# Kernel tuning notes

Measured on AMD Instinct MI355X. Metric: run time of the kernel, lower is better.

The kernel has to match this reference:

```python
import jax, jax.numpy as jnp
import numpy as np

B, T, I, H, O = 512, 512, 128, 50, 10


def setup_inputs() -> dict:
    key = jax.random.key(0)
    ks = jax.random.split(key, 7)
    return {
        "x": jax.random.normal(ks[0], (B, T, I), dtype=jnp.float32),
        "W_ih": jax.random.normal(ks[1], (4 * H, I), dtype=jnp.float32) * 0.05,
        "W_hh": jax.random.normal(ks[2], (4 * H, H), dtype=jnp.float32) * 0.05,
        "b_ih": jax.random.normal(ks[3], (4 * H,), dtype=jnp.float32) * 0.05,
        "b_hh": jax.random.normal(ks[4], (4 * H,), dtype=jnp.float32) * 0.05,
        "W_fc": jax.random.normal(ks[5], (O, H), dtype=jnp.float32) * 0.05,
        "b_fc": jax.random.normal(ks[6], (O,), dtype=jnp.float32) * 0.05,
    }


def reference(x, W_ih, W_hh, b_ih, b_hh, W_fc, b_fc):
    # Single-layer LSTM (PyTorch gate order i,f,g,o), batch_first, zero init state.
    Bsz = x.shape[0]
    Hd = W_hh.shape[1]
    bias = b_ih + b_hh  # [4H]
    # Precompute input projections for all timesteps: [T, B, 4H]
    x_proj = jnp.einsum('bti,gi->tbg', x, W_ih) + bias

    def step(carry, xp_t):
        h, c = carry  # [B, H] each
        gates = xp_t + h @ W_hh.T  # [B, 4H]
        i, f, g, o = jnp.split(gates, 4, axis=-1)
        i = jax.nn.sigmoid(i)
        f = jax.nn.sigmoid(f)
        g = jnp.tanh(g)
        o = jax.nn.sigmoid(o)
        c = f * c + i * g
        h = o * jnp.tanh(c)
        return (h, c), None

    h0 = jnp.zeros((Bsz, Hd), dtype=x.dtype)
    c0 = jnp.zeros((Bsz, Hd), dtype=x.dtype)
    (h_last, _), _ = jax.lax.scan(step, (h0, c0), x_proj)
    return h_last @ W_fc.T + b_fc  # [B, O]
```

## Files before the change

kernel.cpp:

```cpp
#include <hip/hip_runtime.h>


#define BB 512
#define TT 512
#define II 128
#define HH 50
#define GG 200

typedef _Float16 half2v __attribute__((ext_vector_type(2)));
typedef _Float16 half4v __attribute__((ext_vector_type(4)));
typedef _Float16 half8v __attribute__((ext_vector_type(8)));
typedef float float4v __attribute__((ext_vector_type(4)));

#if defined(__has_builtin)
#if __has_builtin(__builtin_amdgcn_fdot2)
#define HAVE_FDOT2 1
#endif
#endif

__device__ __forceinline__ float fdot2f(half2v a, half2v b, float c) {
#ifdef HAVE_FDOT2
    return __builtin_amdgcn_fdot2(a, b, c, false);
#else
    return c + (float)a[0] * (float)b[0] + (float)a[1] * (float)b[1];
#endif
}

__device__ __forceinline__ float fsig(float x) {
    return 1.f / (1.f + __expf(-x));
}
__device__ __forceinline__ float ftanh(float x) {
    return 2.f * fsig(2.f * x) - 1.f;
}

__global__ __launch_bounds__(256) void prep_kernel(
    const float* __restrict__ W_ih, const float* __restrict__ W_hh,
    const float* __restrict__ b_ih, const float* __restrict__ b_hh,
    _Float16* __restrict__ wfrags, _Float16* __restrict__ whh16,
    float* __restrict__ biasv)
{
    int idx = blockIdx.x * 256 + threadIdx.x;
    if (idx < 3328) {
        int lane = idx & 63, kc = (idx >> 6) & 3, nt = idx >> 8;
        int gp = nt * 16 + (lane & 15);
        int k0 = kc * 32 + ((lane >> 4) & 3) * 8;
        half8v v;
        if (gp < GG) {
            int u = gp >> 2, j = gp & 3;
            const float* wr = W_ih + (size_t)(j * HH + u) * II + k0;
            #pragma unroll
            for (int q = 0; q < 8; ++q) v[q] = (_Float16)wr[q];
        } else {
            #pragma unroll
            for (int q = 0; q < 8; ++q) v[q] = (_Float16)0.f;
        }
        *(half8v*)(wfrags + (size_t)idx * 8) = v;
    } else if (idx < 3328 + 2800) {
        int r = idx - 3328;
        int g = r / 14, j4 = r % 14;
        #pragma unroll
        for (int j = 0; j < 4; ++j) {
            int hidx = j4 * 4 + j;
            whh16[g * 56 + hidx] = (hidx < HH) ? (_Float16)W_hh[g * HH + hidx]
                                               : (_Float16)0.f;
        }
    } else if (idx < 3328 + 2800 + GG) {
        int gp = idx - 6128;
        int u = gp >> 2, j = gp & 3;
        biasv[gp] = b_ih[j * HH + u] + b_hh[j * HH + u];
    }
}

__global__ __launch_bounds__(256) void xproj_mfma(
    const float* __restrict__ x, const _Float16* __restrict__ wfrags,
    const float* __restrict__ biasv, _Float16* __restrict__ xp16,
    int t0, int ntile)
{
    __shared__ __align__(16) _Float16 wflds[3328 * 8];
    __shared__ __align__(16) _Float16 dtile[64 * GG];
    __shared__ float blds[GG];
    const int tid = threadIdx.x;
    const int b = blockIdx.x;
    const int w = tid >> 6, l = tid & 63;

    for (int s = tid; s < 3328; s += 256)
        *(float4v*)(wflds + (size_t)s * 8) = *(const float4v*)(wfrags + (size_t)s * 8);
    for (int s = tid; s < GG; s += 256) blds[s] = biasv[s];

    const int row = w * 16 + (l & 15);
    const int kq = (l >> 4) & 3;
    const float* xbase = x + ((size_t)b * TT + (size_t)t0 + row) * II + kq * 8;

    float4 f0[4], f1[4];
    #pragma unroll
    for (int kc = 0; kc < 4; ++kc) {
        f0[kc] = *(const float4*)(xbase + kc * 32);
        f1[kc] = *(const float4*)(xbase + kc * 32 + 4);
    }
    __syncthreads();

    const int colb = l & 15, rq = l >> 4;

    for (int tt = 0; tt < ntile; ++tt) {
        half8v a[4];
        #pragma unroll
        for (int kc = 0; kc < 4; ++kc) {
            a[kc][0] = (_Float16)f0[kc].x; a[kc][1] = (_Float16)f0[kc].y;
            a[kc][2] = (_Float16)f0[kc].z; a[kc][3] = (_Float16)f0[kc].w;
            a[kc][4] = (_Float16)f1[kc].x; a[kc][5] = (_Float16)f1[kc].y;
            a[kc][6] = (_Float16)f1[kc].z; a[kc][7] = (_Float16)f1[kc].w;
        }
        if (tt + 1 < ntile) {
            const float* xn = xbase + (size_t)(tt + 1) * 64 * II;
            #pragma unroll
            for (int kc = 0; kc < 4; ++kc) {
                f0[kc] = *(const float4*)(xn + kc * 32);
                f1[kc] = *(const float4*)(xn + kc * 32 + 4);
            }
        }

        float4v acc[13];
        #pragma unroll
        for (int nt = 0; nt < 13; ++nt) acc[nt] = (float4v){0.f, 0.f, 0.f, 0.f};
        #pragma unroll
        for (int kc = 0; kc < 4; ++kc) {
            #pragma unroll
            for (int nt = 0; nt < 13; ++nt) {
                half8v bf = *(const half8v*)(wflds + (size_t)(((nt * 4 + kc) * 64) + l) * 8);
                acc[nt] = __builtin_amdgcn_mfma_f32_16x16x32_f16(a[kc], bf, acc[nt], 0, 0, 0);
            }
        }

        __syncthreads();
        #pragma unroll
        for (int nt = 0; nt < 13; ++nt) {
            int g = nt * 16 + colb;
            if (g < GG) {
                float bs = blds[g];
                #pragma unroll
                for (int reg = 0; reg < 4; ++reg)
                    dtile[(w * 16 + rq * 4 + reg) * GG + g] = (_Float16)(acc[nt][reg] + bs);
            }
        }
        __syncthreads();

        _Float16* outp = xp16 + ((size_t)b * ntile + tt) * 64 * GG;
        #pragma unroll
        for (int it = 0; it < 7; ++it) {
            int idx = it * 256 + tid;
            if (idx < 1600) {
                float4v v = *(const float4v*)(dtile + (size_t)idx * 8);
                *(float4v*)(outp + (size_t)idx * 8) = v;
            }
        }
    }
}

__global__
__attribute__((amdgpu_flat_work_group_size(256, 256)))
__attribute__((amdgpu_waves_per_eu(1, 2)))
void lstm_rec(
    const _Float16* __restrict__ xp16, const _Float16* __restrict__ whh16,
    float* __restrict__ hs, float* __restrict__ cs, int Tc, int first)
{
    __shared__ __align__(16) _Float16 hbuf[56];
    const int b = blockIdx.x;
    const int tid = threadIdx.x;
    const int gp = (tid < GG) ? tid : 197;
    const int u = gp >> 2;
    const int gate = gp & 3;
    const int wrow = gate * HH + u;

    float4v wv[7];
    #pragma unroll
    for (int j = 0; j < 7; ++j)
        wv[j] = *(const float4v*)(whh16 + (size_t)wrow * 56 + j * 8);

    float c = (!first) ? cs[b * HH + u] : 0.f;

    if (tid < 56)
        hbuf[tid] = (tid < HH && !first) ? (_Float16)hs[b * HH + tid]
                                         : (_Float16)0.f;
    __syncthreads();

    const _Float16* xpb = xp16 + (size_t)b * Tc * GG + gp;
    _Float16 xpf = xpb[0];

    float hlast = 0.f;
    for (int t = 0; t < Tc; ++t) {
        int tn = (t + 1 < Tc) ? t + 1 : t;
        _Float16 xnew = xpb[(size_t)tn * GG];

        float4v hv[7];
        #pragma unroll
        for (int j = 0; j < 7; ++j) hv[j] = *(const float4v*)(hbuf + j * 8);

        float a0 = 0.f, a1 = 0.f, a2 = 0.f, a3 = 0.f;
        #pragma unroll
        for (int j = 0; j < 7; ++j) {
            const half2v* hp = (const half2v*)&hv[j];
            const half2v* wp = (const half2v*)&wv[j];
            a0 = fdot2f(hp[0], wp[0], a0);
            a1 = fdot2f(hp[1], wp[1], a1);
            a2 = fdot2f(hp[2], wp[2], a2);
            a3 = fdot2f(hp[3], wp[3], a3);
        }
        float acc = ((a0 + a1) + (a2 + a3)) + (float)xpf;

        bool isg = (gate == 2);
        float xin = isg ? 2.f * acc : acc;
        float sg = fsig(xin);
        float act = isg ? (2.f * sg - 1.f) : sg;

        int ai = __builtin_bit_cast(int, act);
        float gi = __builtin_bit_cast(float, __builtin_amdgcn_mov_dpp(ai, 0x00, 0xF, 0xF, true));
        float gf = __builtin_bit_cast(float, __builtin_amdgcn_mov_dpp(ai, 0x55, 0xF, 0xF, true));
        float gg = __builtin_bit_cast(float, __builtin_amdgcn_mov_dpp(ai, 0xAA, 0xF, 0xF, true));
        float go = __builtin_bit_cast(float, __builtin_amdgcn_mov_dpp(ai, 0xFF, 0xF, 0xF, true));

        c = gf * c + gi * gg;
        float hn = go * ftanh(c);

        if (tid < GG && gate == 0) hbuf[u] = (_Float16)hn;
        __syncthreads();

        xpf = xnew;
        hlast = hn;
    }

    if (tid < GG && gate == 0) {
        hs[b * HH + u] = hlast;
        cs[b * HH + u] = c;
    }
}

__global__ __launch_bounds__(256) void fc_kernel(
    const float* __restrict__ hs, const float* __restrict__ W_fc,
    const float* __restrict__ b_fc, float* __restrict__ out)
{
    int idx = blockIdx.x * blockDim.x + threadIdx.x;
    if (idx < BB * 10) {
        int b = idx / 10, o = idx % 10;
        float a = b_fc[o];
        #pragma unroll
        for (int kx = 0; kx < HH; ++kx)
            a += hs[b * HH + kx] * W_fc[o * HH + kx];
        out[idx] = a;
    }
}

extern "C" void kernel_launch(void* const* d_in, const int* in_sizes, int n_in,
                              void* d_out, int out_size, void* d_ws, size_t ws_size,
                              hipStream_t stream)
{
    const float* x    = (const float*)d_in[0];
    const float* W_ih = (const float*)d_in[1];
    const float* W_hh = (const float*)d_in[2];
    const float* b_ih = (const float*)d_in[3];
    const float* b_hh = (const float*)d_in[4];
    const float* W_fc = (const float*)d_in[5];
    const float* b_fc = (const float*)d_in[6];
    float* out = (float*)d_out;
    char* wsb = (char*)d_ws;

    const size_t hs_b = (size_t)BB * HH * sizeof(float);
    const size_t wfrags_b = (size_t)13 * 4 * 64 * 8 * 2;
    const size_t whh_b = (size_t)GG * 56 * 2;
    const size_t bias_b = 1024;
    const size_t fixed_b = 2 * hs_b + wfrags_b + whh_b + bias_b;

    int Tc = TT;
    while (Tc > 64 && (size_t)BB * Tc * GG * 2 + fixed_b > ws_size)
        Tc >>= 1;

    _Float16* xp16 = (_Float16*)wsb;
    char* p = wsb + (size_t)BB * Tc * GG * 2;
    float* hsbuf = (float*)p;            p += hs_b;
    float* csbuf = (float*)p;            p += hs_b;
    _Float16* wfrags = (_Float16*)p;     p += wfrags_b;
    _Float16* whh16 = (_Float16*)p;      p += whh_b;
    float* biasv = (float*)p;

    prep_kernel<<<25, 256, 0, stream>>>(W_ih, W_hh, b_ih, b_hh, wfrags, whh16, biasv);

    const int nch = TT / Tc;
    for (int j = 0; j < nch; ++j) {
        xproj_mfma<<<BB, 256, 0, stream>>>(x, wfrags, biasv, xp16, j * Tc, Tc >> 6);
        lstm_rec<<<BB, 256, 0, stream>>>(xp16, whh16, hsbuf, csbuf, Tc, j == 0);
    }
    fc_kernel<<<(BB * 10 + 255) / 256, 256, 0, stream>>>(hsbuf, W_fc, b_fc, out);
}
```

Before: 434.8 us.

## Double-buffer hidden state, prefetch input projections 4 steps ahead, lighter barrier

Keeps the recurrent hidden state in two shared-memory buffers so each step reads one buffer while the gate-0 threads write the other. This removes the read-after-write hazard within a step. Input projections are now prefetched four timesteps ahead in a small register ring, with the loop unrolled by four, to hide global load latency on the serial recurrence. The __syncthreads is replaced by an inline-asm wait on LDS counters plus s_barrier, so the barrier no longer waits on the outstanding global prefetches. This relies on the asm ordering being correct and adds a few registers.

```diff
diff --git a/kernel.cpp b/kernel.cpp
--- a/kernel.cpp
+++ b/kernel.cpp
@@ -163,7 +163,7 @@
     const _Float16* __restrict__ xp16, const _Float16* __restrict__ whh16,
     float* __restrict__ hs, float* __restrict__ cs, int Tc, int first)
 {
-    __shared__ __align__(16) _Float16 hbuf[56];
+    __shared__ __align__(16) _Float16 hbuf[2][56];
     const int b = blockIdx.x;
     const int tid = threadIdx.x;
     const int gp = (tid < GG) ? tid : 197;
@@ -178,22 +178,36 @@
 
     float c = (!first) ? cs[b * HH + u] : 0.f;
 
-    if (tid < 56)
-        hbuf[tid] = (tid < HH && !first) ? (_Float16)hs[b * HH + tid]
-                                         : (_Float16)0.f;
+    if (tid < 56) {
+        hbuf[0][tid] = (tid < HH && !first) ? (_Float16)hs[b * HH + tid]
+                                            : (_Float16)0.f;
+        hbuf[1][tid] = (_Float16)0.f;
+    }
     __syncthreads();
 
     const _Float16* xpb = xp16 + (size_t)b * Tc * GG + gp;
-    _Float16 xpf = xpb[0];
+    _Float16 pv[4];
+    #pragma unroll
+    for (int d = 0; d < 4; ++d) {
+        int td = (d < Tc) ? d : (Tc - 1);
+        pv[d] = xpb[(size_t)td * GG];
+    }
 
     float hlast = 0.f;
+    #pragma unroll 4
     for (int t = 0; t < Tc; ++t) {
-        int tn = (t + 1 < Tc) ? t + 1 : t;
-        _Float16 xnew = xpb[(size_t)tn * GG];
+        const int s = t & 3;
+        const int p = t & 1;
 
         float4v hv[7];
         #pragma unroll
-        for (int j = 0; j < 7; ++j) hv[j] = *(const float4v*)(hbuf + j * 8);
+        for (int j = 0; j < 7; ++j) hv[j] = *(const float4v*)(hbuf[p] + j * 8);
+
+        float xpf = (float)pv[s];
+        {
+            int tn = t + 4; if (tn >= Tc) tn = Tc - 1;
+            pv[s] = xpb[(size_t)tn * GG];
+        }
 
         float a0 = 0.f, a1 = 0.f, a2 = 0.f, a3 = 0.f;
         #pragma unroll
@@ -205,7 +219,7 @@
             a2 = fdot2f(hp[2], wp[2], a2);
             a3 = fdot2f(hp[3], wp[3], a3);
         }
-        float acc = ((a0 + a1) + (a2 + a3)) + (float)xpf;
+        float acc = ((a0 + a1) + (a2 + a3)) + xpf;
 
         bool isg = (gate == 2);
         float xin = isg ? 2.f * acc : acc;
@@ -221,10 +235,9 @@
         c = gf * c + gi * gg;
         float hn = go * ftanh(c);
 
-        if (tid < GG && gate == 0) hbuf[u] = (_Float16)hn;
-        __syncthreads();
-
-        xpf = xnew;
+        if (tid < GG && gate == 0) hbuf[p ^ 1][u] = (_Float16)hn;
+        asm volatile("s_waitcnt lgkmcnt(0)\n\ts_barrier" ::: "memory");
+
         hlast = hn;
     }
 
```

Result: no change. 439.8 us (+1.2%).
